# Kernel tuning notes

Measured on AMD Instinct MI355X. Metric: run time of the kernel, lower is better.

## Reference

```python
import jax, jax.numpy as jnp
import numpy as np

B, T, C, H = 2, 2048, 1024, 16
D = C // H  # head dim


def setup_inputs() -> dict:
    key = jax.random.key(0)
    ks = jax.random.split(key, 10)
    s = 1.0 / np.sqrt(C)  # xavier-ish scale
    inp = {
        "q": jax.random.normal(ks[0], (B, T, C), jnp.float32),
        "k": jax.random.normal(ks[1], (B, T, C), jnp.float32),
        "Wq": jax.random.normal(ks[2], (C, C), jnp.float32) * s,
        "bq": jnp.zeros((C,), jnp.float32),
        "Wk": jax.random.normal(ks[3], (C, C), jnp.float32) * s,
        "bk": jnp.zeros((C,), jnp.float32),
        "Wv": jax.random.normal(ks[4], (C, C), jnp.float32) * s,
        "bv": jnp.zeros((C,), jnp.float32),
        "Wo": jax.random.normal(ks[5], (C, C), jnp.float32) * s,
        "bo": jnp.zeros((C,), jnp.float32),
        # causal mask (lower triangular); masked_fill where mask == 0
        "mask": jnp.tril(jnp.ones((T, T), jnp.int32))[None, None],
    }
    return inp


def reference(q, k, Wq, bq, Wk, bk, Wv, bv, Wo, bo, mask):
    # projections (weights stored input-major: y = x @ W + b)
    qp = q @ Wq + bq                       # [B,T,C]
    kp = k @ Wk + bk                       # [B,T,C]
    vp = kp @ Wv + bv                      # quirk: V computed from projected K

    def heads(x):
        return x.reshape(B, T, H, D).transpose(0, 2, 1, 3)  # [B,H,T,D]

    qh, kh, vh = heads(qp), heads(kp), heads(vp)
    scores = jnp.einsum("bhqd,bhkd->bhqk", qh, kh) / jnp.sqrt(jnp.float32(D))
    scores = jnp.where(mask == 0, -jnp.inf, scores)
    attention_weights = jax.nn.softmax(scores, axis=-1)  # [B,H,T,T]
    # dropout omitted (eval mode / p=0)
    ctx = jnp.einsum("bhqk,bhkd->bhqd", attention_weights, vh)
    ctx = ctx.transpose(0, 2, 1, 3).reshape(B, T, C)
    out = ctx @ Wo + bo
    return out, attention_weights
```

## Files before the change

### kernel.cpp

```cpp
#include <hip/hip_runtime.h>

typedef __attribute__((ext_vector_type(8))) short bf16x8;
typedef __attribute__((ext_vector_type(4))) float f32x4;
typedef unsigned short u16;
typedef unsigned int u32;

#define T_SEQ 2048
#define C_DIM 1024
#define NH 16
#define HD 64
#define BATCH 2

__device__ __forceinline__ u16 f2bf(float f) {
    union { float f; u32 u; } v; v.f = f;
    u32 u = v.u;
    u32 r = (u + 0x7FFFu + ((u >> 16) & 1u)) >> 16;
    return (u16)r;
}

__device__ __forceinline__ float fexp2(float x) { return __builtin_amdgcn_exp2f(x); }

__device__ __forceinline__ float bflo(u32 u) {
    union { u32 u; float f; } v; v.u = u << 16; return v.f;
}
__device__ __forceinline__ float bfhi(u32 u) {
    union { u32 u; float f; } v; v.u = u & 0xFFFF0000u; return v.f;
}

__device__ __forceinline__ void gld_lds16(const void* g, void* l) {
    __builtin_amdgcn_global_load_lds(
        (const __attribute__((address_space(1))) void*)g,
        (__attribute__((address_space(3))) void*)l, 16, 0, 0);
}

__global__ __launch_bounds__(256) void transpose_to_bf16(
    const float* __restrict__ W0, const float* __restrict__ W1,
    const float* __restrict__ W2, const float* __restrict__ W3,
    u16* __restrict__ O0, u16* __restrict__ O1,
    u16* __restrict__ O2, u16* __restrict__ O3)
{
    __shared__ float tile[32][33];
    const float* W = blockIdx.z == 0 ? W0 : blockIdx.z == 1 ? W1 : blockIdx.z == 2 ? W2 : W3;
    u16* O = blockIdx.z == 0 ? O0 : blockIdx.z == 1 ? O1 : blockIdx.z == 2 ? O2 : O3;
    const int tx = threadIdx.x, ty = threadIdx.y;
    const int bx = blockIdx.x * 32, by = blockIdx.y * 32;
#pragma unroll
    for (int i = 0; i < 4; ++i)
        tile[ty + i * 8][tx] = W[(size_t)(by + ty + i * 8) * C_DIM + bx + tx];
    __syncthreads();
#pragma unroll
    for (int i = 0; i < 4; ++i)
        O[(size_t)(bx + ty + i * 8) * C_DIM + by + tx] = f2bf(tile[tx][ty + i * 8]);
}

template<bool XF32, int OMODE>
__global__ __launch_bounds__(256) void gemm_bt(
    const void* __restrict__ X0_, const void* __restrict__ X1_,
    const u16* __restrict__ W0T, const u16* __restrict__ W1T,
    const float* __restrict__ b0_, const float* __restrict__ b1_,
    void* __restrict__ Y0_, void* __restrict__ Y1_,
    int M, int N, int K)
{
    __shared__ u16 As[64 * 32];
    __shared__ u16 Bs[128 * 32];
    const int tid = threadIdx.x;
    const int w = tid >> 6, l = tid & 63;
    const int lr = l & 15, lg = l >> 4;
    const int z = blockIdx.z;
    const void* Xv = z ? X1_ : X0_;
    const u16* WT = z ? W1T : W0T;
    const float* bias = z ? b1_ : b0_;
    void* Yv = z ? Y1_ : Y0_;
    const int m0 = blockIdx.y * 64, n0 = blockIdx.x * 128;
    const int grow = l >> 2, gcol = (l & 3) * 8;
    f32x4 acc[4][2] = {};

    for (int k0 = 0; k0 < K; k0 += 32) {
        __syncthreads();
        if (XF32) {
            const int row = tid >> 2, cg = tid & 3;
            const float* g = (const float*)Xv + (size_t)(m0 + row) * K + k0 + cg * 8;
            float4 a0 = *(const float4*)g;
            float4 a1 = *(const float4*)(g + 4);
            union { u16 h[8]; uint4 q; } pk;
            pk.h[0] = f2bf(a0.x); pk.h[1] = f2bf(a0.y);
            pk.h[2] = f2bf(a0.z); pk.h[3] = f2bf(a0.w);
            pk.h[4] = f2bf(a1.x); pk.h[5] = f2bf(a1.y);
            pk.h[6] = f2bf(a1.z); pk.h[7] = f2bf(a1.w);
            *(uint4*)&As[row * 32 + cg * 8] = pk.q;
        } else {
            gld_lds16((const u16*)Xv + (size_t)(m0 + w * 16 + grow) * K + k0 + gcol,
                      &As[w * 512]);
        }
#pragma unroll
        for (int i = 0; i < 2; ++i)
            gld_lds16(WT + (size_t)(n0 + w * 32 + i * 16 + grow) * K + k0 + gcol,
                      &Bs[(w * 2 + i) * 512]);
        __syncthreads();
        bf16x8 af[4], bfr[2];
#pragma unroll
        for (int i = 0; i < 4; ++i)
            af[i] = *(const bf16x8*)&As[(i * 16 + lr) * 32 + lg * 8];
#pragma unroll
        for (int j = 0; j < 2; ++j)
            bfr[j] = *(const bf16x8*)&Bs[(w * 32 + j * 16 + lr) * 32 + lg * 8];
#pragma unroll
        for (int i = 0; i < 4; ++i)
#pragma unroll
            for (int j = 0; j < 2; ++j)
                acc[i][j] = __builtin_amdgcn_mfma_f32_16x16x32_bf16(af[i], bfr[j], acc[i][j], 0, 0, 0);
    }

#pragma unroll
    for (int i = 0; i < 4; ++i) {
        const int rowb = m0 + i * 16 + lg * 4;
#pragma unroll
        for (int j = 0; j < 2; ++j) {
            const int col = n0 + w * 32 + j * 16 + lr;
            const float bv = bias[col];
            if (OMODE == 2) {
                union { u16 h[4]; uint2 q; } pk;
#pragma unroll
                for (int r = 0; r < 4; ++r) pk.h[r] = f2bf(acc[i][j][r] + bv);
                const int bb = rowb >> 11, tt = rowb & 2047;
                const int hh = col >> 6, dd = col & 63;
                u16* dst = (u16*)Yv + ((size_t)((bb * NH + hh) * HD + dd)) * T_SEQ + tt;
                *(uint2*)dst = pk.q;
            } else {
#pragma unroll
                for (int r = 0; r < 4; ++r) {
                    const float v = acc[i][j][r] + bv;
                    if (OMODE == 1)
                        ((float*)Yv)[(size_t)(rowb + r) * N + col] = v;
                    else
                        ((u16*)Yv)[(size_t)(rowb + r) * N + col] = f2bf(v);
                }
            }
        }
    }
}

#define PV_QS 67
#define PV_WS (16 * PV_QS + 8)

__global__ __launch_bounds__(512, 4) void attn_kernel(
    const u16* __restrict__ qp, const u16* __restrict__ kp,
    const u16* __restrict__ vt, u16* __restrict__ ctx,
    float* __restrict__ attn)
{
    __shared__ float statm[8][16], statl[8][16];
    __shared__ float pvbuf[8 * PV_WS];
    __shared__ float pchunk[8][16][68];

    const int tid = threadIdx.x;
    const int w = tid >> 6, l = tid & 63;
    const int lr = l & 15, lg = l >> 4;

    const int wgid = (blockIdx.x & 7) * 512 + (blockIdx.x >> 3);
    const int b = wgid >> 11;
    const int h = (wgid >> 7) & 15;
    const int strip = 127 - (wgid & 127);
    const int q0 = strip * 16;

    const size_t bh_off = (size_t)b * T_SEQ * C_DIM + h * HD;
    const u16* qb = qp + bh_off;
    const u16* kb = kp + bh_off;
    const u16* vtb = vt + ((size_t)(b * NH + h) * HD) * T_SEQ;
    float* ab = attn + (size_t)(b * NH + h) * T_SEQ * T_SEQ;

    const float SC = 0.125f * 1.44269504088896f;
    const float MNEG = -1e30f;

    const int qrow = q0 + lr;
    const int nt = (q0 + 47) >> 5;
    const int lo = (w * nt) >> 3;
    const int hi = ((w + 1) * nt) >> 3;

    {
        const int zs = nt * 32;
        const int row = tid >> 5;
        const int c0 = (tid & 31) * 4;
        float* zr = ab + (size_t)(q0 + row) * T_SEQ;
        const f32x4 z4 = { 0.f, 0.f, 0.f, 0.f };
        for (int c = zs + c0; c < T_SEQ; c += 128)
            __builtin_nontemporal_store(z4, (f32x4*)(zr + c));
    }

    const bf16x8 aq0 = *(const bf16x8*)(qb + (size_t)(q0 + lr) * C_DIM + lg * 8);
    const bf16x8 aq1 = *(const bf16x8*)(qb + (size_t)(q0 + lr) * C_DIM + 32 + lg * 8);

    u32 ec[8][2];
    u32 ec2[8][2];
    float mtj[8], Sj[8];
    float ml = MNEG;
#pragma unroll
    for (int jj = 0; jj < 8; ++jj) {
        const int ti = lo + jj;
        if (ti < hi) {
            const int kvb = ti * 32;
            const u16* kr0 = kb + (size_t)(kvb + lr) * C_DIM;
            const u16* kr1 = kb + (size_t)(kvb + 16 + lr) * C_DIM;
            const bf16x8 k00 = *(const bf16x8*)(kr0 + lg * 8);
            const bf16x8 k01 = *(const bf16x8*)(kr0 + 32 + lg * 8);
            const bf16x8 k10 = *(const bf16x8*)(kr1 + lg * 8);
            const bf16x8 k11 = *(const bf16x8*)(kr1 + 32 + lg * 8);
            f32x4 s[2] = {};
            s[0] = __builtin_amdgcn_mfma_f32_16x16x32_bf16(k00, aq0, s[0], 0, 0, 0);
            s[0] = __builtin_amdgcn_mfma_f32_16x16x32_bf16(k01, aq1, s[0], 0, 0, 0);
            s[1] = __builtin_amdgcn_mfma_f32_16x16x32_bf16(k10, aq0, s[1], 0, 0, 0);
            s[1] = __builtin_amdgcn_mfma_f32_16x16x32_bf16(k11, aq1, s[1], 0, 0, 0);
            float sv[2][4];
            float mt = MNEG;
#pragma unroll
            for (int t = 0; t < 2; ++t)
#pragma unroll
                for (int r = 0; r < 4; ++r) {
                    float v = s[t][r] * SC;
                    if (kvb + 16 * t + 4 * lg + r > qrow) v = MNEG;
                    sv[t][r] = v;
                    mt = fmaxf(mt, v);
                }
            mtj[jj] = mt;
            float ss = 0.f;
            float e[2][4];
#pragma unroll
            for (int t = 0; t < 2; ++t)
#pragma unroll
                for (int r = 0; r < 4; ++r) {
                    e[t][r] = fexp2(sv[t][r] - mt);
                    ss += e[t][r];
                }
            Sj[jj] = ss;
#pragma unroll
            for (int t = 0; t < 2; ++t) {
                ec[jj][t]  = (u32)f2bf(e[t][0]) | ((u32)f2bf(e[t][1]) << 16);
                ec2[jj][t] = (u32)f2bf(e[t][2]) | ((u32)f2bf(e[t][3]) << 16);
            }
            ml = fmaxf(ml, mt);
        } else {
            mtj[jj] = MNEG; Sj[jj] = 0.f;
            ec[jj][0] = ec[jj][1] = ec2[jj][0] = ec2[jj][1] = 0;
        }
    }
    float ll = 0.f;
#pragma unroll
    for (int jj = 0; jj < 8; ++jj) ll += Sj[jj] * fexp2(mtj[jj] - ml);
#pragma unroll
    for (int d = 16; d <= 32; d <<= 1) {
        const float mo = __shfl_xor(ml, d);
        const float lo2 = __shfl_xor(ll, d);
        const float mn = fmaxf(ml, mo);
        ll = ll * fexp2(ml - mn) + lo2 * fexp2(mo - mn);
        ml = mn;
    }
    if (l < 16) { statm[w][lr] = ml; statl[w][lr] = ll; }
    __syncthreads();

    float mf = MNEG;
#pragma unroll
    for (int ww = 0; ww < 8; ++ww) mf = fmaxf(mf, statm[ww][lr]);
    float lf = 0.f;
#pragma unroll
    for (int ww = 0; ww < 8; ++ww) lf += statl[ww][lr] * fexp2(statm[ww][lr] - mf);
    const float rlf = 1.f / lf;

    f32x4 cacc[4] = {};
#pragma unroll
    for (int j0 = 0; j0 < 8; j0 += 2) {
        int nv = 0;
#pragma unroll
        for (int c = 0; c < 2; ++c) {
            const int jj = j0 + c;
            const int ti = lo + jj;
            if (ti < hi) {
                nv = c + 1;
                const int kvb = ti * 32;
                bf16x8 vf[4];
#pragma unroll
                for (int dt = 0; dt < 4; ++dt)
                    vf[dt] = *(const bf16x8*)(vtb + (size_t)(dt * 16 + lr) * T_SEQ + kvb + lg * 8);
                const float scale = fexp2(mtj[jj] - mf) * rlf;
                u32 pw[2][2];
#pragma unroll
                for (int t2 = 0; t2 < 2; ++t2) {
                    float p[4];
                    p[0] = bflo(ec[jj][t2]) * scale;
                    p[1] = bfhi(ec[jj][t2]) * scale;
                    p[2] = bflo(ec2[jj][t2]) * scale;
                    p[3] = bfhi(ec2[jj][t2]) * scale;
                    f32x4 pv4 = { p[0], p[1], p[2], p[3] };
                    *(f32x4*)&pchunk[w][lr][c * 32 + 16 * t2 + 4 * lg] = pv4;
                    pw[t2][0] = (u32)f2bf(p[0]) | ((u32)f2bf(p[1]) << 16);
                    pw[t2][1] = (u32)f2bf(p[2]) | ((u32)f2bf(p[3]) << 16);
                }
                const int bl = lr + ((lg & 1) << 5);
                const u32 a0 = (u32)__shfl((int)pw[0][0], bl);
                const u32 a1 = (u32)__shfl((int)pw[0][1], bl);
                const u32 a2 = (u32)__shfl((int)pw[0][0], bl + 16);
                const u32 a3 = (u32)__shfl((int)pw[0][1], bl + 16);
                const u32 b0 = (u32)__shfl((int)pw[1][0], bl);
                const u32 b1 = (u32)__shfl((int)pw[1][1], bl);
                const u32 b2 = (u32)__shfl((int)pw[1][0], bl + 16);
                const u32 b3 = (u32)__shfl((int)pw[1][1], bl + 16);
                const bool hi2 = lg >= 2;
                union { u32 ww[4]; bf16x8 v; } pa;
                pa.ww[0] = hi2 ? b0 : a0;
                pa.ww[1] = hi2 ? b1 : a1;
                pa.ww[2] = hi2 ? b2 : a2;
                pa.ww[3] = hi2 ? b3 : a3;
                __builtin_amdgcn_s_setprio(1);
#pragma unroll
                for (int dt = 0; dt < 4; ++dt)
                    cacc[dt] = __builtin_amdgcn_mfma_f32_16x16x32_bf16(pa.v, vf[dt], cacc[dt], 0, 0, 0);
                __builtin_amdgcn_s_setprio(0);
            }
        }
        if (nv) {
            asm volatile("s_waitcnt lgkmcnt(0)" ::: "memory");
            const int colbase = (lo + j0) * 32;
            if (nv == 2) {
#pragma unroll
                for (int i = 0; i < 4; ++i) {
                    const int row = i * 4 + (l >> 4);
                    const int col = (l & 15) * 4;
                    const f32x4 v = *(const f32x4*)&pchunk[w][row][col];
                    __builtin_nontemporal_store(v,
                        (f32x4*)(ab + (size_t)(q0 + row) * T_SEQ + colbase + col));
                }
            } else {
#pragma unroll
                for (int i = 0; i < 2; ++i) {
                    const int row = i * 8 + (l >> 3);
                    const int col = (l & 7) * 4;
                    const f32x4 v = *(const f32x4*)&pchunk[w][row][col];
                    __builtin_nontemporal_store(v,
                        (f32x4*)(ab + (size_t)(q0 + row) * T_SEQ + colbase + col));
                }
            }
        }
    }

    {
        float* pwv = pvbuf + w * PV_WS;
#pragma unroll
        for (int dt = 0; dt < 4; ++dt)
#pragma unroll
            for (int r = 0; r < 4; ++r)
                pwv[(4 * lg + r) * PV_QS + dt * 16 + lr] = cacc[dt][r];
    }
    __syncthreads();

    {
        const int qq = tid >> 5;
        const int d0 = (tid & 31) * 2;
        float s0 = 0.f, s1 = 0.f;
#pragma unroll
        for (int ww = 0; ww < 8; ++ww) {
            const float* pwv = pvbuf + ww * PV_WS + qq * PV_QS;
            s0 += pwv[d0];
            s1 += pwv[d0 + 1];
        }
        union { u16 hh[2]; u32 u; } pk;
        pk.hh[0] = f2bf(s0); pk.hh[1] = f2bf(s1);
        u16* cb = ctx + bh_off;
        *(u32*)(cb + (size_t)(q0 + qq) * C_DIM + d0) = pk.u;
    }
}

extern "C" void kernel_launch(void* const* d_in, const int* in_sizes, int n_in,
                              void* d_out, int out_size, void* d_ws, size_t ws_size,
                              hipStream_t stream)
{
    const float* q  = (const float*)d_in[0];
    const float* k  = (const float*)d_in[1];
    const float* Wq = (const float*)d_in[2];
    const float* bq = (const float*)d_in[3];
    const float* Wk = (const float*)d_in[4];
    const float* bk = (const float*)d_in[5];
    const float* Wv = (const float*)d_in[6];
    const float* bv = (const float*)d_in[7];
    const float* Wo = (const float*)d_in[8];
    const float* bo = (const float*)d_in[9];
    (void)in_sizes; (void)n_in; (void)out_size; (void)ws_size;

    float* out = (float*)d_out;
    float* attn = out + (size_t)BATCH * T_SEQ * C_DIM;

    const size_t MC = (size_t)BATCH * T_SEQ * C_DIM;
    u16* qp  = (u16*)d_ws;
    u16* kp  = qp + MC;
    u16* vt  = kp + MC;
    u16* ctx = vt + MC;
    u16* WqT = ctx + MC;
    u16* WkT = WqT + (size_t)C_DIM * C_DIM;
    u16* WvT = WkT + (size_t)C_DIM * C_DIM;
    u16* WoT = WvT + (size_t)C_DIM * C_DIM;

    transpose_to_bf16<<<dim3(32, 32, 4), dim3(32, 8), 0, stream>>>(
        Wq, Wk, Wv, Wo, WqT, WkT, WvT, WoT);

    const int M = BATCH * T_SEQ;
    dim3 gqk(C_DIM / 128, M / 64, 2);
    dim3 g1(C_DIM / 128, M / 64, 1);
    gemm_bt<true, 0><<<gqk, 256, 0, stream>>>(q, k, WqT, WkT, bq, bk,
                                              qp, kp, M, C_DIM, C_DIM);
    gemm_bt<false, 2><<<g1, 256, 0, stream>>>(kp, kp, WvT, WvT, bv, bv,
                                              vt, vt, M, C_DIM, C_DIM);

    attn_kernel<<<dim3(4096), 512, 0, stream>>>(qp, kp, vt, ctx, attn);

    gemm_bt<false, 1><<<g1, 256, 0, stream>>>(ctx, ctx, WoT, WoT, bo, bo,
                                              out, out, M, C_DIM, C_DIM);
}
```

Measured before the change: 250.2 us.

## Fold Wk·Wv into one weight so V projection runs alongside Q and K

Precomputes Wkv = Wk @ Wv and bkv = bk @ Wv + bv, so V can be computed directly from the raw k input rather than from the projected K. This removes the serial dependency between the K projection and the V projection, letting all three projections run in a single launch over three z-slices. The GEMM K-step is also widened from 32 to 64 to halve the number of barriers. In exchange it adds a weight-product GEMM and a bias kernel on every call, and it changes rounding, since V no longer passes through a bf16 rounding of kp.

```diff
diff --git a/kernel.cpp b/kernel.cpp
--- a/kernel.cpp
+++ b/kernel.cpp
@@ -37,7 +37,8 @@
     const float* __restrict__ W0, const float* __restrict__ W1,
     const float* __restrict__ W2, const float* __restrict__ W3,
     u16* __restrict__ O0, u16* __restrict__ O1,
-    u16* __restrict__ O2, u16* __restrict__ O3)
+    u16* __restrict__ O2, u16* __restrict__ O3,
+    u16* __restrict__ O1b)
 {
     __shared__ float tile[32][33];
     const float* W = blockIdx.z == 0 ? W0 : blockIdx.z == 1 ? W1 : blockIdx.z == 2 ? W2 : W3;
@@ -51,66 +52,149 @@
 #pragma unroll
     for (int i = 0; i < 4; ++i)
         O[(size_t)(bx + ty + i * 8) * C_DIM + by + tx] = f2bf(tile[tx][ty + i * 8]);
-}
-
-template<bool XF32, int OMODE>
+    if (blockIdx.z == 1) {
+#pragma unroll
+        for (int i = 0; i < 4; ++i)
+            O1b[(size_t)(by + ty + i * 8) * C_DIM + bx + tx] = f2bf(tile[ty + i * 8][tx]);
+    }
+}
+
+__global__ __launch_bounds__(256) void bkv_kernel(
+    const float* __restrict__ bk, const float* __restrict__ Wv,
+    const float* __restrict__ bv, float* __restrict__ bkv)
+{
+    const int n = blockIdx.x * 256 + threadIdx.x;
+    float s = bv[n];
+#pragma unroll 4
+    for (int c = 0; c < C_DIM; ++c)
+        s += bk[c] * Wv[(size_t)c * C_DIM + n];
+    bkv[n] = s;
+}
+
+template<int OMODE>
 __global__ __launch_bounds__(256) void gemm_bt(
-    const void* __restrict__ X0_, const void* __restrict__ X1_,
-    const u16* __restrict__ W0T, const u16* __restrict__ W1T,
-    const float* __restrict__ b0_, const float* __restrict__ b1_,
-    void* __restrict__ Y0_, void* __restrict__ Y1_,
+    const u16* __restrict__ Xv, const u16* __restrict__ WT,
+    const float* __restrict__ bias, void* __restrict__ Yv,
     int M, int N, int K)
 {
-    __shared__ u16 As[64 * 32];
-    __shared__ u16 Bs[128 * 32];
+    __shared__ u16 As[64 * 64];
+    __shared__ u16 Bs[128 * 64];
+    const int tid = threadIdx.x;
+    const int w = tid >> 6, l = tid & 63;
+    const int lr = l & 15, lg = l >> 4;
+    const int m0 = blockIdx.y * 64, n0 = blockIdx.x * 128;
+    const int grow8 = l >> 3, gcol8 = (l & 7) * 8;
+    f32x4 acc[4][2] = {};
+
+    for (int k0 = 0; k0 < K; k0 += 64) {
+        __syncthreads();
+#pragma unroll
+        for (int i = 0; i < 2; ++i)
+            gld_lds16(Xv + (size_t)(m0 + w * 16 + i * 8 + grow8) * K + k0 + gcol8,
+                      &As[(w * 16 + i * 8) * 64]);
+#pragma unroll
+        for (int i = 0; i < 4; ++i)
+            gld_lds16(WT + (size_t)(n0 + w * 32 + i * 8 + grow8) * K + k0 + gcol8,
+                      &Bs[(w * 32 + i * 8) * 64]);
+        __syncthreads();
+#pragma unroll
+        for (int hh = 0; hh < 2; ++hh) {
+            bf16x8 af[4], bfr[2];
+#pragma unroll
+            for (int i = 0; i < 4; ++i)
+                af[i] = *(const bf16x8*)&As[(i * 16 + lr) * 64 + hh * 32 + lg * 8];
+#pragma unroll
+            for (int j = 0; j < 2; ++j)
+                bfr[j] = *(const bf16x8*)&Bs[(w * 32 + j * 16 + lr) * 64 + hh * 32 + lg * 8];
+#pragma unroll
+            for (int i = 0; i < 4; ++i)
+#pragma unroll
+                for (int j = 0; j < 2; ++j)
+                    acc[i][j] = __builtin_amdgcn_mfma_f32_16x16x32_bf16(af[i], bfr[j], acc[i][j], 0, 0, 0);
+        }
+    }
+
+#pragma unroll
+    for (int i = 0; i < 4; ++i) {
+        const int rowb = m0 + i * 16 + lg * 4;
+#pragma unroll
+        for (int j = 0; j < 2; ++j) {
+            const int col = n0 + w * 32 + j * 16 + lr;
+            const float bv = (OMODE == 3) ? 0.f : bias[col];
+#pragma unroll
+            for (int r = 0; r < 4; ++r) {
+                const float v = acc[i][j][r] + bv;
+                if (OMODE == 1)
+                    ((float*)Yv)[(size_t)(rowb + r) * N + col] = v;
+                else
+                    ((u16*)Yv)[(size_t)(rowb + r) * N + col] = f2bf(v);
+            }
+        }
+    }
+}
+
+__global__ __launch_bounds__(256) void proj3_kernel(
+    const float* __restrict__ q, const float* __restrict__ k,
+    const u16* __restrict__ WqT, const u16* __restrict__ WkT,
+    const u16* __restrict__ WkvT,
+    const float* __restrict__ bq, const float* __restrict__ bk,
+    const float* __restrict__ bkv,
+    u16* __restrict__ qp, u16* __restrict__ kp, u16* __restrict__ vt)
+{
+    __shared__ u16 As[64 * 64];
+    __shared__ u16 Bs[128 * 64];
     const int tid = threadIdx.x;
     const int w = tid >> 6, l = tid & 63;
     const int lr = l & 15, lg = l >> 4;
     const int z = blockIdx.z;
-    const void* Xv = z ? X1_ : X0_;
-    const u16* WT = z ? W1T : W0T;
-    const float* bias = z ? b1_ : b0_;
-    void* Yv = z ? Y1_ : Y0_;
+    const float* Xv = (z == 0) ? q : k;
+    const u16* WT = (z == 0) ? WqT : (z == 1) ? WkT : WkvT;
+    const float* bias = (z == 0) ? bq : (z == 1) ? bk : bkv;
     const int m0 = blockIdx.y * 64, n0 = blockIdx.x * 128;
-    const int grow = l >> 2, gcol = (l & 3) * 8;
+    const int grow8 = l >> 3, gcol8 = (l & 7) * 8;
+    const int rowA = tid >> 2, cgA = tid & 3;
+    const int K = C_DIM;
     f32x4 acc[4][2] = {};
 
-    for (int k0 = 0; k0 < K; k0 += 32) {
+    for (int k0 = 0; k0 < K; k0 += 64) {
         __syncthreads();
-        if (XF32) {
-            const int row = tid >> 2, cg = tid & 3;
-            const float* g = (const float*)Xv + (size_t)(m0 + row) * K + k0 + cg * 8;
+        {
+            const float* g = Xv + (size_t)(m0 + rowA) * K + k0 + cgA * 16;
             float4 a0 = *(const float4*)g;
             float4 a1 = *(const float4*)(g + 4);
-            union { u16 h[8]; uint4 q; } pk;
-            pk.h[0] = f2bf(a0.x); pk.h[1] = f2bf(a0.y);
-            pk.h[2] = f2bf(a0.z); pk.h[3] = f2bf(a0.w);
-            pk.h[4] = f2bf(a1.x); pk.h[5] = f2bf(a1.y);
-            pk.h[6] = f2bf(a1.z); pk.h[7] = f2bf(a1.w);
-            *(uint4*)&As[row * 32 + cg * 8] = pk.q;
-        } else {
-            gld_lds16((const u16*)Xv + (size_t)(m0 + w * 16 + grow) * K + k0 + gcol,
-                      &As[w * 512]);
-        }
-#pragma unroll
-        for (int i = 0; i < 2; ++i)
-            gld_lds16(WT + (size_t)(n0 + w * 32 + i * 16 + grow) * K + k0 + gcol,
-                      &Bs[(w * 2 + i) * 512]);
+            float4 a2 = *(const float4*)(g + 8);
+            float4 a3 = *(const float4*)(g + 12);
+            union { u16 h[8]; uint4 qv; } p0, p1;
+            p0.h[0] = f2bf(a0.x); p0.h[1] = f2bf(a0.y); p0.h[2] = f2bf(a0.z); p0.h[3] = f2bf(a0.w);
+            p0.h[4] = f2bf(a1.x); p0.h[5] = f2bf(a1.y); p0.h[6] = f2bf(a1.z); p0.h[7] = f2bf(a1.w);
+            p1.h[0] = f2bf(a2.x); p1.h[1] = f2bf(a2.y); p1.h[2] = f2bf(a2.z); p1.h[3] = f2bf(a2.w);
+            p1.h[4] = f2bf(a3.x); p1.h[5] = f2bf(a3.y); p1.h[6] = f2bf(a3.z); p1.h[7] = f2bf(a3.w);
+            *(uint4*)&As[rowA * 64 + cgA * 16] = p0.qv;
+            *(uint4*)&As[rowA * 64 + cgA * 16 + 8] = p1.qv;
+        }
+#pragma unroll
+        for (int i = 0; i < 4; ++i)
+            gld_lds16(WT + (size_t)(n0 + w * 32 + i * 8 + grow8) * K + k0 + gcol8,
+                      &Bs[(w * 32 + i * 8) * 64]);
         __syncthreads();
-        bf16x8 af[4], bfr[2];
-#pragma unroll
-        for (int i = 0; i < 4; ++i)
-            af[i] = *(const bf16x8*)&As[(i * 16 + lr) * 32 + lg * 8];
-#pragma unroll
-        for (int j = 0; j < 2; ++j)
-            bfr[j] = *(const bf16x8*)&Bs[(w * 32 + j * 16 + lr) * 32 + lg * 8];
-#pragma unroll
-        for (int i = 0; i < 4; ++i)
+#pragma unroll
+        for (int hh = 0; hh < 2; ++hh) {
+            bf16x8 af[4], bfr[2];
+#pragma unroll
+            for (int i = 0; i < 4; ++i)
+                af[i] = *(const bf16x8*)&As[(i * 16 + lr) * 64 + hh * 32 + lg * 8];
 #pragma unroll
             for (int j = 0; j < 2; ++j)
-                acc[i][j] = __builtin_amdgcn_mfma_f32_16x16x32_bf16(af[i], bfr[j], acc[i][j], 0, 0, 0);
-    }
-
+                bfr[j] = *(const bf16x8*)&Bs[(w * 32 + j * 16 + lr) * 64 + hh * 32 + lg * 8];
+#pragma unroll
+            for (int i = 0; i < 4; ++i)
+#pragma unroll
+                for (int j = 0; j < 2; ++j)
+                    acc[i][j] = __builtin_amdgcn_mfma_f32_16x16x32_bf16(af[i], bfr[j], acc[i][j], 0, 0, 0);
+        }
+    }
+
+    u16* Yv = (z == 0) ? qp : (z == 1) ? kp : vt;
 #pragma unroll
     for (int i = 0; i < 4; ++i) {
         const int rowb = m0 + i * 16 + lg * 4;
@@ -118,23 +202,18 @@
         for (int j = 0; j < 2; ++j) {
             const int col = n0 + w * 32 + j * 16 + lr;
             const float bv = bias[col];
-            if (OMODE == 2) {
-                union { u16 h[4]; uint2 q; } pk;
+            if (z == 2) {
+                union { u16 h[4]; uint2 qv; } pk;
 #pragma unroll
                 for (int r = 0; r < 4; ++r) pk.h[r] = f2bf(acc[i][j][r] + bv);
                 const int bb = rowb >> 11, tt = rowb & 2047;
-                const int hh = col >> 6, dd = col & 63;
-                u16* dst = (u16*)Yv + ((size_t)((bb * NH + hh) * HD + dd)) * T_SEQ + tt;
-                *(uint2*)dst = pk.q;
+                const int hhh = col >> 6, dd = col & 63;
+                u16* dst = Yv + ((size_t)((bb * NH + hhh) * HD + dd)) * T_SEQ + tt;
+                *(uint2*)dst = pk.qv;
             } else {
 #pragma unroll
-                for (int r = 0; r < 4; ++r) {
-                    const float v = acc[i][j][r] + bv;
-                    if (OMODE == 1)
-                        ((float*)Yv)[(size_t)(rowb + r) * N + col] = v;
-                    else
-                        ((u16*)Yv)[(size_t)(rowb + r) * N + col] = f2bf(v);
-                }
+                for (int r = 0; r < 4; ++r)
+                    Yv[(size_t)(rowb + r) * C_DIM + col] = f2bf(acc[i][j][r] + bv);
             }
         }
     }
@@ -189,8 +268,7 @@
     const bf16x8 aq0 = *(const bf16x8*)(qb + (size_t)(q0 + lr) * C_DIM + lg * 8);
     const bf16x8 aq1 = *(const bf16x8*)(qb + (size_t)(q0 + lr) * C_DIM + 32 + lg * 8);
 
-    u32 ec[8][2];
-    u32 ec2[8][2];
+    u32 ec[8][2], ec2[8][2];
     float mtj[8], Sj[8];
     float ml = MNEG;
 #pragma unroll
@@ -387,28 +465,33 @@
     float* attn = out + (size_t)BATCH * T_SEQ * C_DIM;
 
     const size_t MC = (size_t)BATCH * T_SEQ * C_DIM;
-    u16* qp  = (u16*)d_ws;
-    u16* kp  = qp + MC;
-    u16* vt  = kp + MC;
-    u16* ctx = vt + MC;
-    u16* WqT = ctx + MC;
-    u16* WkT = WqT + (size_t)C_DIM * C_DIM;
-    u16* WvT = WkT + (size_t)C_DIM * C_DIM;
-    u16* WoT = WvT + (size_t)C_DIM * C_DIM;
+    const size_t CC = (size_t)C_DIM * C_DIM;
+    u16* qp   = (u16*)d_ws;
+    u16* kp   = qp + MC;
+    u16* vt   = kp + MC;
+    u16* ctx  = vt + MC;
+    u16* WqT  = ctx + MC;
+    u16* WkT  = WqT + CC;
+    u16* WvT  = WkT + CC;
+    u16* WoT  = WvT + CC;
+    u16* Wkbf = WoT + CC;
+    u16* WkvT = Wkbf + CC;
+    float* bkv = (float*)(WkvT + CC);
 
     transpose_to_bf16<<<dim3(32, 32, 4), dim3(32, 8), 0, stream>>>(
-        Wq, Wk, Wv, Wo, WqT, WkT, WvT, WoT);
+        Wq, Wk, Wv, Wo, WqT, WkT, WvT, WoT, Wkbf);
+
+    bkv_kernel<<<dim3(4), 256, 0, stream>>>(bk, Wv, bv, bkv);
+
+    gemm_bt<3><<<dim3(C_DIM / 128, C_DIM / 64), 256, 0, stream>>>(
+        WvT, Wkbf, bq, WkvT, C_DIM, C_DIM, C_DIM);
 
     const int M = BATCH * T_SEQ;
-    dim3 gqk(C_DIM / 128, M / 64, 2);
-    dim3 g1(C_DIM / 128, M / 64, 1);
-    gemm_bt<true, 0><<<gqk, 256, 0, stream>>>(q, k, WqT, WkT, bq, bk,
-                                              qp, kp, M, C_DIM, C_DIM);
-    gemm_bt<false, 2><<<g1, 256, 0, stream>>>(kp, kp, WvT, WvT, bv, bv,
-                                              vt, vt, M, C_DIM, C_DIM);
+    proj3_kernel<<<dim3(C_DIM / 128, M / 64, 3), 256, 0, stream>>>(
+        q, k, WqT, WkT, WkvT, bq, bk, bkv, qp, kp, vt);
 
     attn_kernel<<<dim3(4096), 512, 0, stream>>>(qp, kp, vt, ctx, attn);
 
-    gemm_bt<false, 1><<<g1, 256, 0, stream>>>(ctx, ctx, WoT, WoT, bo, bo,
-                                              out, out, M, C_DIM, C_DIM);
-}
+    gemm_bt<1><<<dim3(C_DIM / 128, M / 64), 256, 0, stream>>>(
+        ctx, WoT, bo, out, M, C_DIM, C_DIM);
+}
```

Result: slower. 355.8 us (+42.2%).
